# Kernel optimization log

Measured on AMD Instinct MI355X. Metric: run time of the kernel, lower is better.

Reference implementation:

```python
import jax, jax.numpy as jnp
import numpy as np

E = 1024
H = 16
D = E // H  # head_dim = 64


def setup_inputs() -> dict:
    key = jax.random.key(0)
    k_x, k_w1, k_b1, k_w2, k_b2 = jax.random.split(key, 5)
    s = 1.0 / np.sqrt(E)
    return {
        "x": jax.random.normal(k_x, (2, 2048, E), dtype=jnp.float32),
        "qkv_w": jax.random.uniform(k_w1, (3 * E, E), jnp.float32, -s, s),
        "qkv_b": jax.random.uniform(k_b1, (3 * E,), jnp.float32, -s, s),
        "out_w": jax.random.uniform(k_w2, (E, E), jnp.float32, -s, s),
        "out_b": jax.random.uniform(k_b2, (E,), jnp.float32, -s, s),
    }


def reference(x, qkv_w, qkv_b, out_w, out_b):
    B, T, _ = x.shape
    # qkv projection (torch Linear: x @ W.T + b)
    qkv = x @ qkv_w.T + qkv_b  # [B, T, 3E]
    q, k, v = jnp.split(qkv, 3, axis=-1)
    # [B, T, E] -> [B, H, T, D]
    def to_heads(t):
        return t.reshape(B, T, H, D).transpose(0, 2, 1, 3)
    q, k, v = to_heads(q), to_heads(k), to_heads(v)
    scale = 1.0 / np.sqrt(D).astype(np.float32)
    scores = jnp.einsum("bhqd,bhkd->bhqk", q, k) * scale  # [B, H, T, T]
    attn = jax.nn.softmax(scores, axis=-1)
    # dropout is identity in eval mode
    out = jnp.einsum("bhqk,bhkd->bhqd", attn, v)  # [B, H, T, D]
    out = out.transpose(0, 2, 1, 3).reshape(B, T, E)
    return out @ out_w.T + out_b
```

## Files before the change

### kernel.cpp

```cpp
#include <hip/hip_runtime.h>

#define TT 2048
#define BB 2
#define EE 1024
#define HH 16
#define DD 64
#define E3 3072
#define NTOK 4096

typedef unsigned short u16;
typedef _Float16 __attribute__((ext_vector_type(8))) half8;
typedef __fp16 __attribute__((ext_vector_type(2))) fp16x2;
typedef __attribute__((ext_vector_type(4))) float f32x4;

__device__ __forceinline__ unsigned f2h(float f) {
    union { _Float16 h; u16 u; } v; v.h = (_Float16)f; return (unsigned)v.u;
}
__device__ __forceinline__ unsigned pkh(float a, float b) {
    union { fp16x2 h; unsigned u; } v;
    v.h = __builtin_amdgcn_cvt_pkrtz(a, b);
    return v.u;
}

__device__ __forceinline__ void async_ld16(const u16* g, const u16* l) {
    auto gp = reinterpret_cast<const __attribute__((address_space(1))) unsigned*>(
        reinterpret_cast<uintptr_t>(g));
    auto lp = reinterpret_cast<__attribute__((address_space(3))) unsigned*>(
        reinterpret_cast<uintptr_t>(l));
    __builtin_amdgcn_global_load_lds(gp, lp, 16, 0, 0);
}

__global__ __launch_bounds__(256) void split3(
    const float* __restrict__ x, const float* __restrict__ w1,
    const float* __restrict__ w2,
    u16* __restrict__ xh, u16* __restrict__ w1h, u16* __restrict__ w2h)
{
    const int N1 = (NTOK * EE) / 4;
    const int N2 = N1 + (E3 * EE) / 4;
    int i = blockIdx.x * 256 + threadIdx.x;
    const float* src; u16* dst; int j;
    if (i < N1)      { src = x;  dst = xh;  j = i; }
    else if (i < N2) { src = w1; dst = w1h; j = i - N1; }
    else             { src = w2; dst = w2h; j = i - N2; }
    float4 v = ((const float4*)src)[j];
    *(uint2*)&dst[(size_t)j * 4] = make_uint2(
        f2h(v.x) | (f2h(v.y) << 16), f2h(v.z) | (f2h(v.w) << 16));
}

__global__ __launch_bounds__(256) void vtrans(
    const u16* __restrict__ qkv, u16* __restrict__ vt)
{
    __shared__ u16 L[64][72];
    const int tid = threadIdx.x;
    const int t0 = blockIdx.x * 64;
    const int h  = blockIdx.y;
    const int b  = blockIdx.z;
    const int row = tid >> 2;
    const int c16 = (tid & 3) << 4;

    const u16* src = qkv + (size_t)(b * TT + t0 + row) * E3 + 2 * EE + h * DD + c16;
    *(uint4*)&L[row][c16]     = *(const uint4*)src;
    *(uint4*)&L[row][c16 + 8] = *(const uint4*)(src + 8);
    __syncthreads();

    union { uint4 u[2]; u16 s[16]; } P;
#pragma unroll
    for (int j = 0; j < 16; ++j) P.s[j] = L[c16 + j][row];
    u16* dst = vt + ((size_t)(b * HH + h) * DD + row) * TT + t0 + c16;
    *(uint4*)dst       = P.u[0];
    *(uint4*)(dst + 8) = P.u[1];
}

template <int WMT, bool QSCALE, bool F16OUT>
__global__ __launch_bounds__(256, 3) void gemm_f16(
    const u16* __restrict__ Ag, const u16* __restrict__ Wg,
    const float* __restrict__ bias, void* __restrict__ Cout, int M, int N)
{
    constexpr int BM = WMT * 32;
    constexpr int APASS = BM / 32;
    __shared__ u16 sA[BM * 64];
    __shared__ u16 sB[128 * 64];

    const int tid  = threadIdx.x;
    const int lane = tid & 63;
    const int wave = tid >> 6;
    const int quad = lane >> 4;
    const int l16  = lane & 15;
    const int wm = wave >> 1, wn = wave & 1;
    const int m0 = blockIdx.y * BM;
    const int n0 = blockIdx.x * 128;

    const int srow = tid >> 3;
    const int schk = tid & 7;

    const u16* ag[APASS]; int aldw[APASS];
#pragma unroll
    for (int p = 0; p < APASS; ++p) {
        int row = p * 32 + srow;
        ag[p] = Ag + (size_t)(m0 + row) * EE + ((schk ^ (row & 7)) << 3);
        aldw[p] = (p * 256 + wave * 64) * 8;
    }
    const u16* bg[4]; int bldw[4];
#pragma unroll
    for (int p = 0; p < 4; ++p) {
        int row = p * 32 + srow;
        bg[p] = Wg + (size_t)(n0 + row) * EE + ((schk ^ (row & 7)) << 3);
        bldw[p] = (p * 256 + wave * 64) * 8;
    }

    f32x4 acc[WMT][4];
#pragma unroll
    for (int mt = 0; mt < WMT; ++mt)
#pragma unroll
        for (int nt = 0; nt < 4; ++nt) acc[mt][nt] = (f32x4){0.f, 0.f, 0.f, 0.f};

    for (int k0 = 0; k0 < EE; k0 += 64) {
        __syncthreads();
#pragma unroll
        for (int p = 0; p < APASS; ++p) async_ld16(ag[p] + k0, sA + aldw[p]);
#pragma unroll
        for (int p = 0; p < 4; ++p)    async_ld16(bg[p] + k0, sB + bldw[p]);
        __syncthreads();

        half8 fa[WMT][2], fb[4][2];
#pragma unroll
        for (int mt = 0; mt < WMT; ++mt) {
            int r = wm * (WMT * 16) + mt * 16 + l16;
#pragma unroll
            for (int ks = 0; ks < 2; ++ks)
                fa[mt][ks] = *(const half8*)&sA[r * 64 + (((ks * 4 + quad) ^ (r & 7)) << 3)];
        }
#pragma unroll
        for (int nt = 0; nt < 4; ++nt) {
            int r = wn * 64 + nt * 16 + l16;
#pragma unroll
            for (int ks = 0; ks < 2; ++ks)
                fb[nt][ks] = *(const half8*)&sB[r * 64 + (((ks * 4 + quad) ^ (r & 7)) << 3)];
        }
#pragma unroll
        for (int ks = 0; ks < 2; ++ks)
#pragma unroll
            for (int mt = 0; mt < WMT; ++mt)
#pragma unroll
                for (int nt = 0; nt < 4; ++nt)
                    acc[mt][nt] = __builtin_amdgcn_mfma_f32_16x16x32_f16(
                        fa[mt][ks], fb[nt][ks], acc[mt][nt], 0, 0, 0);
    }

    const float scale = (QSCALE && n0 < EE) ? 0.18033688011112042f : 1.0f;
    float bv[4];
#pragma unroll
    for (int nt = 0; nt < 4; ++nt) bv[nt] = bias[n0 + wn * 64 + nt * 16 + l16];
#pragma unroll
    for (int mt = 0; mt < WMT; ++mt)
#pragma unroll
        for (int nt = 0; nt < 4; ++nt)
#pragma unroll
            for (int r = 0; r < 4; ++r) {
                int rg = m0 + wm * (WMT * 16) + mt * 16 + quad * 4 + r;
                int cg = n0 + wn * 64 + nt * 16 + l16;
                float v = (acc[mt][nt][r] + bv[nt]) * scale;
                if (F16OUT) ((u16*)Cout)[(size_t)rg * N + cg] = (u16)f2h(v);
                else        ((float*)Cout)[(size_t)rg * N + cg] = v;
            }
}

__global__ __launch_bounds__(256, 4) void attn_mfma(
    const u16* __restrict__ qkv, const u16* __restrict__ vt,
    u16* __restrict__ obuf)
{
    __shared__ u16 KB[2][64][64];
    __shared__ u16 VB[2][64][64];
    __shared__ u16 QP[64][64];

    const int tid  = threadIdx.x;
    const int wave = tid >> 6;
    const int lane = tid & 63;
    const int quad = lane >> 4;
    const int l16  = lane & 15;

    const int q0 = blockIdx.x * 64;
    const int hh = blockIdx.y;
    const int b  = blockIdx.z;

    const int srow = tid >> 3;
    const int schk = tid & 7;
    const int ldsw = wave * 512;

#pragma unroll
    for (int p = 0; p < 2; ++p) {
        int row = p * 32 + srow;
        const u16* qg = qkv + (size_t)(b * TT + q0 + row) * E3 + hh * DD
                        + ((schk ^ (row & 7)) << 3);
        async_ld16(qg, &QP[0][0] + p * 2048 + ldsw);
    }
#pragma unroll
    for (int p = 0; p < 2; ++p) {
        int row = p * 32 + srow;
        int sw8 = (schk ^ (row & 7)) << 3;
        async_ld16(qkv + (size_t)(b * TT + row) * E3 + EE + hh * DD + sw8,
                   &KB[0][0][0] + p * 2048 + ldsw);
        async_ld16(vt + ((size_t)(b * HH + hh) * DD + row) * TT + sw8,
                   &VB[0][0][0] + p * 2048 + ldsw);
    }
    __syncthreads();

    half8 qb[2];
    {
        int row = wave * 16 + l16;
#pragma unroll
        for (int ks = 0; ks < 2; ++ks)
            qb[ks] = *(const half8*)&QP[row][((ks * 4 + quad) ^ (row & 7)) << 3];
    }

    const f32x4 Z = {0.f, 0.f, 0.f, 0.f};
    float l_i = 0.f;
    f32x4 o[4];
#pragma unroll
    for (int dt = 0; dt < 4; ++dt) o[dt] = (f32x4){0.f, 0.f, 0.f, 0.f};

    int cur = 0;
    for (int kt = 0; kt < TT; kt += 64, cur ^= 1) {
        const int ktn = (kt + 64) & (TT - 1);
#pragma unroll
        for (int p = 0; p < 2; ++p) {
            int row = p * 32 + srow;
            int sw8 = (schk ^ (row & 7)) << 3;
            async_ld16(qkv + (size_t)(b * TT + ktn + row) * E3 + EE + hh * DD + sw8,
                       &KB[cur ^ 1][0][0] + p * 2048 + ldsw);
            async_ld16(vt + ((size_t)(b * HH + hh) * DD + row) * TT + ktn + sw8,
                       &VB[cur ^ 1][0][0] + p * 2048 + ldsw);
        }

        f32x4 s[4];
#pragma unroll
        for (int nt = 0; nt < 4; ++nt) {
            int r0 = nt * 16 + l16;
            half8 kf0 = *(const half8*)&KB[cur][r0][((quad)     ^ (r0 & 7)) << 3];
            half8 kf1 = *(const half8*)&KB[cur][r0][((4 + quad) ^ (r0 & 7)) << 3];
            f32x4 t = __builtin_amdgcn_mfma_f32_16x16x32_f16(kf0, qb[0], Z, 0, 0, 0);
            s[nt] = __builtin_amdgcn_mfma_f32_16x16x32_f16(kf1, qb[1], t, 0, 0, 0);
        }

        {
            int prow = wave * 16 + l16;
            float rs0 = 0.f, rs1 = 0.f;
#pragma unroll
            for (int nt = 0; nt < 4; ++nt) {
                float p0 = __builtin_amdgcn_exp2f(s[nt][0]);
                float p1 = __builtin_amdgcn_exp2f(s[nt][1]);
                float p2 = __builtin_amdgcn_exp2f(s[nt][2]);
                float p3 = __builtin_amdgcn_exp2f(s[nt][3]);
                rs0 += p0 + p1;
                rs1 += p2 + p3;
                int phys = (nt * 2 + (quad >> 1)) ^ (prow & 7);
                *(uint2*)&QP[prow][phys * 8 + ((quad & 1) << 2)] =
                    make_uint2(pkh(p0, p1), pkh(p2, p3));
            }
            l_i += rs0 + rs1;
        }

#pragma unroll
        for (int ks = 0; ks < 2; ++ks) {
            int prow = wave * 16 + l16;
            half8 pf = *(const half8*)&QP[prow][((ks * 4 + quad) ^ (prow & 7)) << 3];
#pragma unroll
            for (int dt = 0; dt < 4; ++dt) {
                int vr = dt * 16 + l16;
                half8 vf = *(const half8*)&VB[cur][vr][((ks * 4 + quad) ^ (vr & 7)) << 3];
                o[dt] = __builtin_amdgcn_mfma_f32_16x16x32_f16(vf, pf, o[dt], 0, 0, 0);
            }
        }

        __syncthreads();
    }

    float inv;
    {
        float l = l_i;
        l += __shfl_xor(l, 16, 64);
        l += __shfl_xor(l, 32, 64);
        inv = 1.f / l;
    }
    {
        size_t base = (size_t)(b * TT + q0 + wave * 16 + l16) * EE + hh * DD;
#pragma unroll
        for (int dt = 0; dt < 4; ++dt) {
            unsigned hv[4];
#pragma unroll
            for (int r = 0; r < 4; ++r) hv[r] = f2h(o[dt][r] * inv);
            *(uint2*)&obuf[base + dt * 16 + quad * 4] =
                make_uint2(hv[0] | (hv[1] << 16), hv[2] | (hv[3] << 16));
        }
    }
}

extern "C" void kernel_launch(void* const* d_in, const int* in_sizes, int n_in,
                              void* d_out, int out_size, void* d_ws, size_t ws_size,
                              hipStream_t stream)
{
    const float* x     = (const float*)d_in[0];
    const float* qkv_w = (const float*)d_in[1];
    const float* qkv_b = (const float*)d_in[2];
    const float* out_w = (const float*)d_in[3];
    const float* out_b = (const float*)d_in[4];
    float* out = (float*)d_out;

    const size_t NX  = (size_t)NTOK * EE;
    const size_t NW1 = (size_t)E3 * EE;
    const size_t NW2 = (size_t)EE * EE;
    const size_t NQ  = (size_t)NTOK * E3;

    u16* ws   = (u16*)d_ws;
    u16* x_h  = ws;
    u16* w1h  = ws + NX;
    u16* w2h  = w1h + NW1;
    u16* qkvb = w2h + NW2;
    u16* vtb  = qkvb + NQ;

    split3<<<dim3((unsigned)((NX + NW1 + NW2) / 4 / 256)), 256, 0, stream>>>(
        x, qkv_w, out_w, x_h, w1h, w2h);

    gemm_f16<4, true, true><<<dim3(E3 / 128, NTOK / 128), 256, 0, stream>>>(
        x_h, w1h, qkv_b, (void*)qkvb, NTOK, E3);

    vtrans<<<dim3(TT / 64, HH, BB), 256, 0, stream>>>(qkvb, vtb);

    attn_mfma<<<dim3(TT / 64, HH, BB), 256, 0, stream>>>(qkvb, vtb, x_h);

    gemm_f16<2, false, false><<<dim3(EE / 128, NTOK / 64), 256, 0, stream>>>(
        x_h, w2h, out_b, (void*)out, NTOK, EE);
}
```

Measured before the change: 190.5 us.

## Fuse V transpose into QKV GEMM epilogue and use per-wave P buffers

```diff
diff --git a/kernel.cpp b/kernel.cpp
--- a/kernel.cpp
+++ b/kernel.cpp
@@ -47,39 +47,17 @@
         f2h(v.x) | (f2h(v.y) << 16), f2h(v.z) | (f2h(v.w) << 16));
 }
 
-__global__ __launch_bounds__(256) void vtrans(
-    const u16* __restrict__ qkv, u16* __restrict__ vt)
-{
-    __shared__ u16 L[64][72];
-    const int tid = threadIdx.x;
-    const int t0 = blockIdx.x * 64;
-    const int h  = blockIdx.y;
-    const int b  = blockIdx.z;
-    const int row = tid >> 2;
-    const int c16 = (tid & 3) << 4;
-
-    const u16* src = qkv + (size_t)(b * TT + t0 + row) * E3 + 2 * EE + h * DD + c16;
-    *(uint4*)&L[row][c16]     = *(const uint4*)src;
-    *(uint4*)&L[row][c16 + 8] = *(const uint4*)(src + 8);
-    __syncthreads();
-
-    union { uint4 u[2]; u16 s[16]; } P;
-#pragma unroll
-    for (int j = 0; j < 16; ++j) P.s[j] = L[c16 + j][row];
-    u16* dst = vt + ((size_t)(b * HH + h) * DD + row) * TT + t0 + c16;
-    *(uint4*)dst       = P.u[0];
-    *(uint4*)(dst + 8) = P.u[1];
-}
-
 template <int WMT, bool QSCALE, bool F16OUT>
 __global__ __launch_bounds__(256, 3) void gemm_f16(
     const u16* __restrict__ Ag, const u16* __restrict__ Wg,
-    const float* __restrict__ bias, void* __restrict__ Cout, int M, int N)
+    const float* __restrict__ bias, void* __restrict__ Cout,
+    u16* __restrict__ vtp, int M, int N)
 {
     constexpr int BM = WMT * 32;
     constexpr int APASS = BM / 32;
-    __shared__ u16 sA[BM * 64];
-    __shared__ u16 sB[128 * 64];
+    __shared__ u16 sAB[(BM + 128) * 64];
+    u16* sA = sAB;
+    u16* sB = sAB + BM * 64;
 
     const int tid  = threadIdx.x;
     const int lane = tid & 63;
@@ -151,6 +129,38 @@
     float bv[4];
 #pragma unroll
     for (int nt = 0; nt < 4; ++nt) bv[nt] = bias[n0 + wn * 64 + nt * 16 + l16];
+
+    if constexpr (F16OUT) {
+        if (vtp != nullptr && n0 >= 2 * EE) {
+            __syncthreads();
+            u16* tile = sAB;
+#pragma unroll
+            for (int mt = 0; mt < WMT; ++mt)
+#pragma unroll
+                for (int nt = 0; nt < 4; ++nt) {
+                    int c  = wn * 64 + nt * 16 + l16;
+                    int ub = (wm * 16 + mt * 4 + quad) ^ ((c & 7) << 1);
+                    *(uint2*)&tile[c * 128 + ub * 4] = make_uint2(
+                        f2h(acc[mt][nt][0] + bv[nt]) | (f2h(acc[mt][nt][1] + bv[nt]) << 16),
+                        f2h(acc[mt][nt][2] + bv[nt]) | (f2h(acc[mt][nt][3] + bv[nt]) << 16));
+                }
+            __syncthreads();
+            const int c    = tid >> 1;
+            const int hf   = tid & 1;
+            const int hd   = ((n0 - 2 * EE) >> 6) + (c >> 6);
+            const int d    = c & 63;
+            const int bq   = m0 >> 11;
+            u16* dst = vtp + ((size_t)(bq * HH + hd) * DD + d) * TT
+                           + (m0 & (TT - 1)) + hf * 64;
+#pragma unroll
+            for (int j = 0; j < 8; ++j) {
+                int u = (hf * 16 + j * 2) ^ ((c & 7) << 1);
+                *(uint4*)(dst + j * 8) = *(const uint4*)&tile[c * 128 + u * 4];
+            }
+            return;
+        }
+    }
+
 #pragma unroll
     for (int mt = 0; mt < WMT; ++mt)
 #pragma unroll
@@ -171,7 +181,7 @@
 {
     __shared__ u16 KB[2][64][64];
     __shared__ u16 VB[2][64][64];
-    __shared__ u16 QP[64][64];
+    __shared__ u16 PB[4][16][64];
 
     const int tid  = threadIdx.x;
     const int wave = tid >> 6;
@@ -187,13 +197,14 @@
     const int schk = tid & 7;
     const int ldsw = wave * 512;
 
-#pragma unroll
-    for (int p = 0; p < 2; ++p) {
-        int row = p * 32 + srow;
-        const u16* qg = qkv + (size_t)(b * TT + q0 + row) * E3 + hh * DD
-                        + ((schk ^ (row & 7)) << 3);
-        async_ld16(qg, &QP[0][0] + p * 2048 + ldsw);
-    }
+    half8 qb[2];
+    {
+        int row = q0 + wave * 16 + l16;
+        const u16* qg = qkv + (size_t)(b * TT + row) * E3 + hh * DD;
+        qb[0] = *(const half8*)(qg + quad * 8);
+        qb[1] = *(const half8*)(qg + 32 + quad * 8);
+    }
+
 #pragma unroll
     for (int p = 0; p < 2; ++p) {
         int row = p * 32 + srow;
@@ -205,19 +216,14 @@
     }
     __syncthreads();
 
-    half8 qb[2];
-    {
-        int row = wave * 16 + l16;
-#pragma unroll
-        for (int ks = 0; ks < 2; ++ks)
-            qb[ks] = *(const half8*)&QP[row][((ks * 4 + quad) ^ (row & 7)) << 3];
-    }
-
     const f32x4 Z = {0.f, 0.f, 0.f, 0.f};
     float l_i = 0.f;
     f32x4 o[4];
 #pragma unroll
     for (int dt = 0; dt < 4; ++dt) o[dt] = (f32x4){0.f, 0.f, 0.f, 0.f};
+
+    const int px = (l16 & 7) << 1;
+    u16* prow = &PB[wave][l16][0];
 
     int cur = 0;
     for (int kt = 0; kt < TT; kt += 64, cur ^= 1) {
@@ -232,42 +238,29 @@
                        &VB[cur ^ 1][0][0] + p * 2048 + ldsw);
         }
 
-        f32x4 s[4];
-#pragma unroll
-        for (int nt = 0; nt < 4; ++nt) {
-            int r0 = nt * 16 + l16;
+#pragma unroll
+        for (int kg = 0; kg < 4; ++kg) {
+            int r0 = kg * 16 + l16;
             half8 kf0 = *(const half8*)&KB[cur][r0][((quad)     ^ (r0 & 7)) << 3];
             half8 kf1 = *(const half8*)&KB[cur][r0][((4 + quad) ^ (r0 & 7)) << 3];
             f32x4 t = __builtin_amdgcn_mfma_f32_16x16x32_f16(kf0, qb[0], Z, 0, 0, 0);
-            s[nt] = __builtin_amdgcn_mfma_f32_16x16x32_f16(kf1, qb[1], t, 0, 0, 0);
-        }
-
-        {
-            int prow = wave * 16 + l16;
-            float rs0 = 0.f, rs1 = 0.f;
-#pragma unroll
-            for (int nt = 0; nt < 4; ++nt) {
-                float p0 = __builtin_amdgcn_exp2f(s[nt][0]);
-                float p1 = __builtin_amdgcn_exp2f(s[nt][1]);
-                float p2 = __builtin_amdgcn_exp2f(s[nt][2]);
-                float p3 = __builtin_amdgcn_exp2f(s[nt][3]);
-                rs0 += p0 + p1;
-                rs1 += p2 + p3;
-                int phys = (nt * 2 + (quad >> 1)) ^ (prow & 7);
-                *(uint2*)&QP[prow][phys * 8 + ((quad & 1) << 2)] =
-                    make_uint2(pkh(p0, p1), pkh(p2, p3));
-            }
-            l_i += rs0 + rs1;
-        }
-
-#pragma unroll
-        for (int ks = 0; ks < 2; ++ks) {
-            int prow = wave * 16 + l16;
-            half8 pf = *(const half8*)&QP[prow][((ks * 4 + quad) ^ (prow & 7)) << 3];
+            f32x4 s = __builtin_amdgcn_mfma_f32_16x16x32_f16(kf1, qb[1], t, 0, 0, 0);
+            float p0 = __builtin_amdgcn_exp2f(s[0]);
+            float p1 = __builtin_amdgcn_exp2f(s[1]);
+            float p2 = __builtin_amdgcn_exp2f(s[2]);
+            float p3 = __builtin_amdgcn_exp2f(s[3]);
+            l_i += (p0 + p1) + (p2 + p3);
+            int pu = (kg * 4 + quad) ^ px;
+            *(uint2*)&prow[pu * 4] = make_uint2(pkh(p0, p1), pkh(p2, p3));
+        }
+
+#pragma unroll
+        for (int kb = 0; kb < 2; ++kb) {
+            half8 pf = *(const half8*)&prow[((kb * 8 + quad * 2) ^ px) << 2];
 #pragma unroll
             for (int dt = 0; dt < 4; ++dt) {
                 int vr = dt * 16 + l16;
-                half8 vf = *(const half8*)&VB[cur][vr][((ks * 4 + quad) ^ (vr & 7)) << 3];
+                half8 vf = *(const half8*)&VB[cur][vr][((kb * 4 + quad) ^ (vr & 7)) << 3];
                 o[dt] = __builtin_amdgcn_mfma_f32_16x16x32_f16(vf, pf, o[dt], 0, 0, 0);
             }
         }
@@ -286,11 +279,10 @@
         size_t base = (size_t)(b * TT + q0 + wave * 16 + l16) * EE + hh * DD;
 #pragma unroll
         for (int dt = 0; dt < 4; ++dt) {
-            unsigned hv[4];
-#pragma unroll
-            for (int r = 0; r < 4; ++r) hv[r] = f2h(o[dt][r] * inv);
+            unsigned h0 = f2h(o[dt][0] * inv), h1 = f2h(o[dt][1] * inv);
+            unsigned h2 = f2h(o[dt][2] * inv), h3 = f2h(o[dt][3] * inv);
             *(uint2*)&obuf[base + dt * 16 + quad * 4] =
-                make_uint2(hv[0] | (hv[1] << 16), hv[2] | (hv[3] << 16));
+                make_uint2(h0 | (h1 << 16), h2 | (h3 << 16));
         }
     }
 }
@@ -322,12 +314,10 @@
         x, qkv_w, out_w, x_h, w1h, w2h);
 
     gemm_f16<4, true, true><<<dim3(E3 / 128, NTOK / 128), 256, 0, stream>>>(
-        x_h, w1h, qkv_b, (void*)qkvb, NTOK, E3);
-
-    vtrans<<<dim3(TT / 64, HH, BB), 256, 0, stream>>>(qkvb, vtb);
+        x_h, w1h, qkv_b, (void*)qkvb, vtb, NTOK, E3);
 
     attn_mfma<<<dim3(TT / 64, HH, BB), 256, 0, stream>>>(qkvb, vtb, x_h);
 
     gemm_f16<2, false, false><<<dim3(EE / 128, NTOK / 64), 256, 0, stream>>>(
-        x_h, w2h, out_b, (void*)out, NTOK, EE);
-}
+        x_h, w2h, out_b, (void*)out, nullptr, NTOK, EE);
+}
```

Result: faster. 183.9 us (-3.5%).
